# Kernel optimization log

Hardware: AMD Instinct MI355X
Metric: run time of the kernel (lower is better)

The kernel has to match this reference:

```python
import jax, jax.numpy as jnp
import numpy as np

B, Z, A, D = 2048, 128, 4, 50000
EPS = 1e-8


def setup_inputs() -> dict:
    key = jax.random.key(0)
    k1, k2, k3, k4, k5 = jax.random.split(key, 5)
    return {
        "batch_x": jax.random.normal(k1, (B, Z), dtype=jnp.float32),
        "batch_next": jax.random.normal(k2, (B, Z), dtype=jnp.float32),
        "keys": jax.random.normal(k3, (A, D, Z), dtype=jnp.float32),
        "vals": jax.random.normal(k4, (A, D, Z), dtype=jnp.float32),
        "batch_a": jax.random.randint(k5, (B,), 0, A, dtype=jnp.int64),
    }


def _dnd_lookup(q, keys_a, vals_a):
    # q: [B, Z] (L2-normalized), keys_a: [D, Z], vals_a: [D, Z]
    kn = keys_a / (jnp.linalg.norm(keys_a, axis=-1, keepdims=True) + EPS)
    sims = jnp.einsum("bz,dz->bd", q, kn)          # cosine similarity [B, D]
    w = jax.nn.softmax(sims, axis=-1)                # attention over dictionary
    return jnp.einsum("bd,dz->bz", w, vals_a)       # [B, Z]


def reference(batch_x, batch_next, keys, vals, batch_a):
    # Per-sample routed DND lookup: each sample queries the memory of its action,
    # then MSE loss vs batch_next (eval-mode trainBatch; memory write is a state
    # mutation done after the loss and does not affect the returned value).
    qn = batch_x / (jnp.linalg.norm(batch_x, axis=-1, keepdims=True) + EPS)
    a_space = keys.shape[0]
    pred = jnp.zeros_like(batch_x)
    for a in range(a_space):  # small fixed loop over distinct memories
        pred_a = _dnd_lookup(qn, keys[a], vals[a])
        pred = jnp.where((batch_a == a)[:, None], pred_a, pred)
    return jnp.mean((pred - batch_next) ** 2)
```

## Files before the change

kernel.cpp:

```cpp
#include <hip/hip_runtime.h>
#include <stdint.h>

#define B_N 2048
#define Z_N 128
#define A_N 4
#define D_N 50000
#define D_PAD 51200
#define EPS_F 1e-8f

#define TILE_B 128
#define KT 32
#define NSPLIT 64
#define SPAN 800
#define NITER 25
#define KL_S 140
#define VL_S 40

#define NORM_BLOCKS 51712
#define VT_BX 800

typedef __attribute__((ext_vector_type(8))) short short8;
typedef __attribute__((ext_vector_type(4))) float f32x4;
typedef __attribute__((ext_vector_type(2))) unsigned int u32x2;

__device__ __forceinline__ unsigned short f2bf(float f) {
  unsigned int u = __builtin_bit_cast(unsigned int, f);
  u += 0x7FFFu + ((u >> 16) & 1u);
  return (unsigned short)(u >> 16);
}

__device__ __forceinline__ void plswap32(unsigned int& a, unsigned int& b) {
#if __has_builtin(__builtin_amdgcn_permlane32_swap)
  u32x2 r = __builtin_amdgcn_permlane32_swap(a, b, false, false);
  a = r[0]; b = r[1];
#else
  asm volatile("v_permlane32_swap_b32 %0, %1" : "+v"(a), "+v"(b));
#endif
}
__device__ __forceinline__ void plswap16(unsigned int& a, unsigned int& b) {
#if __has_builtin(__builtin_amdgcn_permlane16_swap)
  u32x2 r = __builtin_amdgcn_permlane16_swap(a, b, false, false);
  a = r[0]; b = r[1];
#else
  asm volatile("v_permlane16_swap_b32 %0, %1" : "+v"(a), "+v"(b));
#endif
}

__global__ void k_prep(const float* __restrict__ keys, const float* __restrict__ x,
                       const float* __restrict__ vals,
                       unsigned short* __restrict__ kn, unsigned short* __restrict__ qnb,
                       unsigned short* __restrict__ vt) {
  if (blockIdx.x < NORM_BLOCKS) {
    int w = threadIdx.x >> 6, lane = threadIdx.x & 63;
    int row = blockIdx.x * 4 + w;
    const float* src;
    unsigned short* dst;
    if (row >= A_N * D_PAD) {
      int r = row - A_N * D_PAD;
      src = x + (size_t)r * Z_N;
      dst = qnb + (size_t)r * Z_N;
    } else {
      int a = row / D_PAD, d = row - a * D_PAD;
      dst = kn + (size_t)row * Z_N;
      if (d >= D_N) { ((unsigned int*)dst)[lane] = 0u; return; }
      src = keys + ((size_t)a * D_N + d) * Z_N;
    }
    const float2 v = ((const float2*)src)[lane];
    float ss = v.x * v.x + v.y * v.y;
#pragma unroll
    for (int m = 1; m < 64; m <<= 1) ss += __shfl_xor(ss, m);
    float inv = 1.0f / (sqrtf(ss) + EPS_F);
    unsigned int packed = ((unsigned int)f2bf(v.y * inv) << 16) | f2bf(v.x * inv);
    ((unsigned int*)dst)[lane] = packed;
    return;
  }
  __shared__ float tile[64][65];
  int b = blockIdx.x - NORM_BLOCKS;
  int bx = b % VT_BX, rest = b / VT_BX;
  int by = rest & 1, a = rest >> 1;
  int d0 = bx * 64, z0 = by * 64;
  int t = threadIdx.x;
  int r = t >> 4, c4 = (t & 15) * 4;
#pragma unroll
  for (int i = 0; i < 4; ++i) {
    int dr = r + i * 16, d = d0 + dr;
    float4 v = {0.f, 0.f, 0.f, 0.f};
    if (d < D_N) v = *(const float4*)(vals + ((size_t)a * D_N + d) * Z_N + z0 + c4);
    tile[dr][c4 + 0] = v.x; tile[dr][c4 + 1] = v.y;
    tile[dr][c4 + 2] = v.z; tile[dr][c4 + 3] = v.w;
  }
  __syncthreads();
  int zz = t >> 2, dg = (t & 3) * 16;
  union { unsigned short u[16]; uint4 q[2]; } pk;
#pragma unroll
  for (int j = 0; j < 16; ++j) pk.u[j] = f2bf(tile[dg + j][zz]);
  unsigned short* dst = vt + ((size_t)a * Z_N + z0 + zz) * D_PAD + d0 + dg;
  ((uint4*)dst)[0] = pk.q[0];
  ((uint4*)dst)[1] = pk.q[1];
}

__global__ void k_route(const int* __restrict__ act, int* __restrict__ counts,
                        int* __restrict__ lists, int* __restrict__ work) {
  __shared__ int lc[4];
  int t = threadIdx.x;
  if (t < 4) lc[t] = 0;
  __syncthreads();
  for (int i = t; i < B_N; i += 1024) {
    int a = act[i];
    int pos = atomicAdd(&lc[a], 1);
    lists[a * B_N + pos] = i;
  }
  __syncthreads();
  if (t < 4) counts[t] = lc[t];
  int t0 = (lc[0] + TILE_B - 1) >> 7, t1 = (lc[1] + TILE_B - 1) >> 7;
  int t2 = (lc[2] + TILE_B - 1) >> 7, t3 = (lc[3] + TILE_B - 1) >> 7;
  int T = t0 + t1 + t2 + t3;
  int total = T * NSPLIT;
  if (t == 0) work[0] = total;
  for (int i = t; i < total; i += 1024) {
    int lo = i & 7, q = i >> 3;
    int chi = q / T, j = q - chi * T;
    int c = (chi << 3) | lo;
    int a, ty;
    if (j < t0)                { a = 0; ty = j; }
    else if (j < t0 + t1)      { a = 1; ty = j - t0; }
    else if (j < t0 + t1 + t2) { a = 2; ty = j - t0 - t1; }
    else                       { a = 3; ty = j - t0 - t1 - t2; }
    work[1 + i] = a | (ty << 2) | (c << 8);
  }
}

__launch_bounds__(512)
__global__ void k_flash(const unsigned short* __restrict__ kn,
                        const unsigned short* __restrict__ vt,
                        const unsigned short* __restrict__ qnb,
                        const int* __restrict__ counts,
                        const int* __restrict__ lists,
                        const int* __restrict__ work,
                        float* __restrict__ acc,
                        float* __restrict__ sume) {
  int total = work[0];
  if ((int)blockIdx.x >= total) return;
  int wi = work[1 + blockIdx.x];
  int a = wi & 3, ty = (wi >> 2) & 63, span = wi >> 8;
  int nb = counts[a];

  __shared__ unsigned short Kl[2][KT * KL_S];
  __shared__ unsigned short Vl[2][128 * VL_S];

  int t = threadIdx.x;
  int w = t >> 6, lane = t & 63;
  int lq = lane >> 4, ln = lane & 15;

  const unsigned short* kn_a = kn + (size_t)a * D_PAD * Z_N;
  const unsigned short* vt_a = vt + (size_t)a * Z_N * D_PAD;
  const int* list_a = lists + a * B_N;

  int g0 = ty * TILE_B + w * 16 + ln;
  bool qvalid = g0 < nb;
  int si0 = qvalid ? list_a[g0] : 0;
  short8 qf[4];
#pragma unroll
  for (int c = 0; c < 4; ++c) {
    short8 s = (short8){0,0,0,0,0,0,0,0};
    if (qvalid) s = *(const short8*)(qnb + (size_t)si0 * Z_N + c * 32 + lq * 8);
    qf[c] = s;
  }

  f32x4 O[8];
#pragma unroll
  for (int zt = 0; zt < 8; ++zt) O[zt] = (f32x4){0.f, 0.f, 0.f, 0.f};
  float rs = 0.f;

  int d_base = span * SPAN;
  int sk_key = t >> 4, sk_z = (t & 15) * 8;
  int sv_z = t >> 2, sv_k = (t & 3) * 8;

  uint4 kp, vp;

#define LOAD_TILE(d)                                                          \
  {                                                                           \
    kp = *(const uint4*)(kn_a + (size_t)((d) + sk_key) * Z_N + sk_z);         \
    vp = *(const uint4*)(vt_a + (size_t)sv_z * D_PAD + (d) + sv_k);           \
  }
#define STORE_TILE(p)                                                         \
  {                                                                           \
    *(uint4*)&Kl[p][sk_key * KL_S + sk_z] = kp;                               \
    *(uint4*)&Vl[p][sv_z * VL_S + sv_k] = vp;                                 \
  }

  LOAD_TILE(d_base);
  STORE_TILE(0);
  LOAD_TILE(d_base + KT);
  __syncthreads();

  int p = 0;
  for (int kt = 0; kt < NITER; ++kt) {
    int d0 = d_base + kt * KT;
    if (kt + 1 < NITER) {
      STORE_TILE(p ^ 1);
      if (kt + 2 < NITER) LOAD_TILE(d0 + 2 * KT)
    }

    f32x4 ST[2];
    __builtin_amdgcn_s_setprio(1);
#pragma unroll
    for (int nt = 0; nt < 2; ++nt) {
      short8 kf[4];
#pragma unroll
      for (int c = 0; c < 4; ++c)
        kf[c] = *(const short8*)&Kl[p][(nt * 16 + ln) * KL_S + c * 32 + lq * 8];
      f32x4 s4 = (f32x4){0.f, 0.f, 0.f, 0.f};
#pragma unroll
      for (int c = 0; c < 4; ++c)
        s4 = __builtin_amdgcn_mfma_f32_16x16x32_bf16(kf[c], qf[c], s4, 0, 0, 0);
      ST[nt] = s4;
    }
    __builtin_amdgcn_s_setprio(0);

    unsigned int s00, s01, s10, s11;
    {
      float e0 = __expf(ST[0][0]), e1 = __expf(ST[0][1]);
      float e2 = __expf(ST[0][2]), e3 = __expf(ST[0][3]);
      float f0 = __expf(ST[1][0]), f1 = __expf(ST[1][1]);
      float f2 = __expf(ST[1][2]), f3 = __expf(ST[1][3]);
      rs += ((e0 + e1) + (e2 + e3)) + ((f0 + f1) + (f2 + f3));
      asm("v_cvt_pk_bf16_f32 %0, %1, %2" : "=v"(s00) : "v"(e0), "v"(e1));
      asm("v_cvt_pk_bf16_f32 %0, %1, %2" : "=v"(s01) : "v"(e2), "v"(e3));
      asm("v_cvt_pk_bf16_f32 %0, %1, %2" : "=v"(s10) : "v"(f0), "v"(f1));
      asm("v_cvt_pk_bf16_f32 %0, %1, %2" : "=v"(s11) : "v"(f2), "v"(f3));
    }

    plswap32(s00, s10);
    plswap32(s01, s11);
    plswap16(s00, s10);
    plswap16(s01, s11);
    union { unsigned int u[4]; short8 v; } pa;
    pa.u[0] = s00; pa.u[1] = s01; pa.u[2] = s10; pa.u[3] = s11;

    __builtin_amdgcn_s_setprio(1);
#pragma unroll
    for (int zt = 0; zt < 8; ++zt) {
      short8 vf = *(const short8*)&Vl[p][(zt * 16 + ln) * VL_S + lq * 8];
      O[zt] = __builtin_amdgcn_mfma_f32_16x16x32_bf16(pa.v, vf, O[zt], 0, 0, 0);
    }
    __builtin_amdgcn_s_setprio(0);

    __syncthreads();
    p ^= 1;
  }

  rs += __shfl_xor(rs, 16);
  rs += __shfl_xor(rs, 32);

  if (lq == 0 && qvalid) atomicAdd(&sume[si0], rs);
#pragma unroll
  for (int r = 0; r < 4; ++r) {
    int g = ty * TILE_B + w * 16 + lq * 4 + r;
    if (g < nb) {
      int si = list_a[g];
      float* arow = acc + (size_t)si * Z_N + ln;
#pragma unroll
      for (int zt = 0; zt < 8; ++zt) atomicAdd(arow + zt * 16, O[zt][r]);
    }
  }
}

__global__ void k_loss(const float* __restrict__ acc, const float* __restrict__ sume,
                       const float* __restrict__ nxt, float* __restrict__ out) {
  __shared__ float ls[4];
  int w = threadIdx.x >> 6, lane = threadIdx.x & 63;
  int row = blockIdx.x * 4 + w;
  float inv = 1.0f / (sume[row] - (float)(D_PAD - D_N));
  const float2 p2 = ((const float2*)(acc + (size_t)row * Z_N))[lane];
  const float2 n2 = ((const float2*)(nxt + (size_t)row * Z_N))[lane];
  float dx = p2.x * inv - n2.x, dy = p2.y * inv - n2.y;
  float s = dx * dx + dy * dy;
#pragma unroll
  for (int m = 1; m < 64; m <<= 1) s += __shfl_xor(s, m);
  if (lane == 0) ls[w] = s;
  __syncthreads();
  if (threadIdx.x == 0)
    atomicAdd(out, (ls[0] + ls[1] + ls[2] + ls[3]) * (1.0f / (float)(B_N * Z_N)));
}

extern "C" void kernel_launch(void* const* d_in, const int* in_sizes, int n_in,
                              void* d_out, int out_size, void* d_ws, size_t ws_size,
                              hipStream_t stream) {
  const float* x    = (const float*)d_in[0];
  const float* nxt  = (const float*)d_in[1];
  const float* keys = (const float*)d_in[2];
  const float* vals = (const float*)d_in[3];
  const int*   act  = (const int*)d_in[4];

  char* ws = (char*)d_ws;
  float* acc    = (float*)(ws + 0);
  float* sume   = (float*)(ws + 1048576);
  int*   counts = (int*)(ws + 1056784);
  int*   lists  = (int*)(ws + 1056800);
  int*   work   = (int*)(ws + 1089568);
  unsigned short* qnb = (unsigned short*)(ws + 1097760);
  unsigned short* kn  = (unsigned short*)(ws + 1622048);
  unsigned short* vt  = (unsigned short*)(ws + 54050848);

  hipMemsetAsync(ws, 0, 1056784, stream);
  hipMemsetAsync(d_out, 0, 4, stream);

  k_route<<<1, 1024, 0, stream>>>(act, counts, lists, work);
  k_prep<<<NORM_BLOCKS + VT_BX * 2 * A_N, 256, 0, stream>>>(keys, x, vals, kn, qnb, vt);
  k_flash<<<1216, 512, 0, stream>>>(kn, vt, qnb, counts, lists, work, acc, sume);
  k_loss<<<512, 256, 0, stream>>>(acc, sume, nxt, (float*)d_out);
}
```

Measured before the change: 392.9 us.

## Fuse routing into prep kernel, widen row normalization, drop setprio hints

The single-block routing kernel is folded into the prep kernel as one extra trailing block, which removes a kernel launch. Row normalization now has each half-wave process one row with float4 loads, so each block covers 8 rows and the block count is halved. The s_setprio priority hints around the MFMA sections in the flash kernel are also removed. The routing block is the last block scheduled in prep and its loops now stride by 256 threads instead of 1024, but it runs alongside a large amount of other work.

```diff
diff --git a/kernel.cpp b/kernel.cpp
--- a/kernel.cpp
+++ b/kernel.cpp
@@ -16,8 +16,9 @@
 #define KL_S 140
 #define VL_S 40
 
-#define NORM_BLOCKS 51712
+#define NROW_BLOCKS 25856
 #define VT_BX 800
+#define VT_BLOCKS 6400
 
 typedef __attribute__((ext_vector_type(8))) short short8;
 typedef __attribute__((ext_vector_type(4))) float f32x4;
@@ -47,12 +48,16 @@
 }
 
 __global__ void k_prep(const float* __restrict__ keys, const float* __restrict__ x,
-                       const float* __restrict__ vals,
+                       const float* __restrict__ vals, const int* __restrict__ act,
                        unsigned short* __restrict__ kn, unsigned short* __restrict__ qnb,
-                       unsigned short* __restrict__ vt) {
-  if (blockIdx.x < NORM_BLOCKS) {
+                       unsigned short* __restrict__ vt,
+                       int* __restrict__ counts, int* __restrict__ lists,
+                       int* __restrict__ work) {
+  __shared__ float tile[64][65];
+  if (blockIdx.x < NROW_BLOCKS) {
     int w = threadIdx.x >> 6, lane = threadIdx.x & 63;
-    int row = blockIdx.x * 4 + w;
+    int l32 = lane & 31;
+    int row = blockIdx.x * 8 + w * 2 + (lane >> 5);
     const float* src;
     unsigned short* dst;
     if (row >= A_N * D_PAD) {
@@ -62,50 +67,53 @@
     } else {
       int a = row / D_PAD, d = row - a * D_PAD;
       dst = kn + (size_t)row * Z_N;
-      if (d >= D_N) { ((unsigned int*)dst)[lane] = 0u; return; }
+      if (d >= D_N) {
+        ((u32x2*)dst)[l32] = (u32x2){0u, 0u};
+        return;
+      }
       src = keys + ((size_t)a * D_N + d) * Z_N;
     }
-    const float2 v = ((const float2*)src)[lane];
-    float ss = v.x * v.x + v.y * v.y;
-#pragma unroll
-    for (int m = 1; m < 64; m <<= 1) ss += __shfl_xor(ss, m);
+    const float4 v = ((const float4*)src)[l32];
+    float ss = v.x * v.x + v.y * v.y + v.z * v.z + v.w * v.w;
+#pragma unroll
+    for (int m = 1; m < 32; m <<= 1) ss += __shfl_xor(ss, m);
     float inv = 1.0f / (sqrtf(ss) + EPS_F);
-    unsigned int packed = ((unsigned int)f2bf(v.y * inv) << 16) | f2bf(v.x * inv);
-    ((unsigned int*)dst)[lane] = packed;
+    u32x2 pk;
+    pk[0] = ((unsigned int)f2bf(v.y * inv) << 16) | f2bf(v.x * inv);
+    pk[1] = ((unsigned int)f2bf(v.w * inv) << 16) | f2bf(v.z * inv);
+    ((u32x2*)dst)[l32] = pk;
     return;
   }
-  __shared__ float tile[64][65];
-  int b = blockIdx.x - NORM_BLOCKS;
-  int bx = b % VT_BX, rest = b / VT_BX;
-  int by = rest & 1, a = rest >> 1;
-  int d0 = bx * 64, z0 = by * 64;
-  int t = threadIdx.x;
-  int r = t >> 4, c4 = (t & 15) * 4;
-#pragma unroll
-  for (int i = 0; i < 4; ++i) {
-    int dr = r + i * 16, d = d0 + dr;
-    float4 v = {0.f, 0.f, 0.f, 0.f};
-    if (d < D_N) v = *(const float4*)(vals + ((size_t)a * D_N + d) * Z_N + z0 + c4);
-    tile[dr][c4 + 0] = v.x; tile[dr][c4 + 1] = v.y;
-    tile[dr][c4 + 2] = v.z; tile[dr][c4 + 3] = v.w;
-  }
-  __syncthreads();
-  int zz = t >> 2, dg = (t & 3) * 16;
-  union { unsigned short u[16]; uint4 q[2]; } pk;
-#pragma unroll
-  for (int j = 0; j < 16; ++j) pk.u[j] = f2bf(tile[dg + j][zz]);
-  unsigned short* dst = vt + ((size_t)a * Z_N + z0 + zz) * D_PAD + d0 + dg;
-  ((uint4*)dst)[0] = pk.q[0];
-  ((uint4*)dst)[1] = pk.q[1];
-}
-
-__global__ void k_route(const int* __restrict__ act, int* __restrict__ counts,
-                        int* __restrict__ lists, int* __restrict__ work) {
-  __shared__ int lc[4];
+  if (blockIdx.x < NROW_BLOCKS + VT_BLOCKS) {
+    int b = blockIdx.x - NROW_BLOCKS;
+    int bx = b % VT_BX, rest = b / VT_BX;
+    int by = rest & 1, a = rest >> 1;
+    int d0 = bx * 64, z0 = by * 64;
+    int t = threadIdx.x;
+    int r = t >> 4, c4 = (t & 15) * 4;
+#pragma unroll
+    for (int i = 0; i < 4; ++i) {
+      int dr = r + i * 16, d = d0 + dr;
+      float4 v = {0.f, 0.f, 0.f, 0.f};
+      if (d < D_N) v = *(const float4*)(vals + ((size_t)a * D_N + d) * Z_N + z0 + c4);
+      tile[dr][c4 + 0] = v.x; tile[dr][c4 + 1] = v.y;
+      tile[dr][c4 + 2] = v.z; tile[dr][c4 + 3] = v.w;
+    }
+    __syncthreads();
+    int zz = t >> 2, dg = (t & 3) * 16;
+    union { unsigned short u[16]; uint4 q[2]; } pk;
+#pragma unroll
+    for (int j = 0; j < 16; ++j) pk.u[j] = f2bf(tile[dg + j][zz]);
+    unsigned short* dst = vt + ((size_t)a * Z_N + z0 + zz) * D_PAD + d0 + dg;
+    ((uint4*)dst)[0] = pk.q[0];
+    ((uint4*)dst)[1] = pk.q[1];
+    return;
+  }
+  int* lc = (int*)tile;
   int t = threadIdx.x;
   if (t < 4) lc[t] = 0;
   __syncthreads();
-  for (int i = t; i < B_N; i += 1024) {
+  for (int i = t; i < B_N; i += 256) {
     int a = act[i];
     int pos = atomicAdd(&lc[a], 1);
     lists[a * B_N + pos] = i;
@@ -117,7 +125,7 @@
   int T = t0 + t1 + t2 + t3;
   int total = T * NSPLIT;
   if (t == 0) work[0] = total;
-  for (int i = t; i < total; i += 1024) {
+  for (int i = t; i < total; i += 256) {
     int lo = i & 7, q = i >> 3;
     int chi = q / T, j = q - chi * T;
     int c = (chi << 3) | lo;
@@ -203,7 +211,6 @@
     }
 
     f32x4 ST[2];
-    __builtin_amdgcn_s_setprio(1);
 #pragma unroll
     for (int nt = 0; nt < 2; ++nt) {
       short8 kf[4];
@@ -216,7 +223,6 @@
         s4 = __builtin_amdgcn_mfma_f32_16x16x32_bf16(kf[c], qf[c], s4, 0, 0, 0);
       ST[nt] = s4;
     }
-    __builtin_amdgcn_s_setprio(0);
 
     unsigned int s00, s01, s10, s11;
     {
@@ -238,13 +244,11 @@
     union { unsigned int u[4]; short8 v; } pa;
     pa.u[0] = s00; pa.u[1] = s01; pa.u[2] = s10; pa.u[3] = s11;
 
-    __builtin_amdgcn_s_setprio(1);
 #pragma unroll
     for (int zt = 0; zt < 8; ++zt) {
       short8 vf = *(const short8*)&Vl[p][(zt * 16 + ln) * VL_S + lq * 8];
       O[zt] = __builtin_amdgcn_mfma_f32_16x16x32_bf16(pa.v, vf, O[zt], 0, 0, 0);
     }
-    __builtin_amdgcn_s_setprio(0);
 
     __syncthreads();
     p ^= 1;
@@ -306,8 +310,8 @@
   hipMemsetAsync(ws, 0, 1056784, stream);
   hipMemsetAsync(d_out, 0, 4, stream);
 
-  k_route<<<1, 1024, 0, stream>>>(act, counts, lists, work);
-  k_prep<<<NORM_BLOCKS + VT_BX * 2 * A_N, 256, 0, stream>>>(keys, x, vals, kn, qnb, vt);
+  k_prep<<<NROW_BLOCKS + VT_BLOCKS + 1, 256, 0, stream>>>(
+      keys, x, vals, act, kn, qnb, vt, counts, lists, work);
   k_flash<<<1216, 512, 0, stream>>>(kn, vt, qnb, counts, lists, work, acc, sume);
   k_loss<<<512, 256, 0, stream>>>(acc, sume, nxt, (float*)d_out);
 }
```

Measured after the change: 365.7 us. -6.9%, faster.
